# Performance work log

Measured on AMD Instinct MI355X. Metric: run time of the kernel, lower is better.

## Reference

```python
import math
import jax, jax.numpy as jnp
import numpy as np

D_SCALES = 4  # MSGAD d parameter


def calc_thetas(d):
    # Numeric replication of calculate_theta2 (beta-wavelet polynomial coeffs).
    # p_i(x) = (x/2)^i (1 - x/2)^(d-i) / (2 * Beta(i+1, d+1-i)); keep the d
    # lowest-order coefficients (constant .. x^{d-1}), matching the original.
    thetas = []
    for i in range(d):
        beta = math.factorial(i) * math.factorial(d - i) / math.factorial(d + 1)
        p = (np.poly1d([0.5, 0.0]) ** i) * (np.poly1d([-0.5, 1.0]) ** (d - i)) / (2.0 * beta)
        c = p.coeffs  # highest degree first, length d+1
        thetas.append([float(c[d - j]) for j in range(d)])
    return thetas

THETAS = calc_thetas(D_SCALES)


def setup_inputs() -> dict:
    key = jax.random.key(0)
    k1, k2, k3, k4 = jax.random.split(key, 4)
    N, E, IN, H = 8192, 262144, 256, 128
    in_feat = jax.random.normal(k1, (N, IN), dtype=jnp.float32)
    W = jax.random.normal(k2, (IN, H), dtype=jnp.float32) * 0.05
    b = jnp.zeros((H,), dtype=jnp.float32)
    src = jax.random.randint(k3, (E,), 0, N, dtype=jnp.int32)
    dst = jax.random.randint(k4, (E,), 0, N, dtype=jnp.int32)
    return {"in_feat": in_feat, "W": W, "b": b, "src": src, "dst": dst}


def reference(in_feat, W, b, src, dst):
    N = in_feat.shape[0]
    # Linear + LeakyReLU encoder
    h = jax.nn.leaky_relu(in_feat @ W + b, negative_slope=0.01)
    # dgl.add_self_loop
    loop = jnp.arange(N, dtype=src.dtype)
    s = jnp.concatenate([src, loop])
    d_ = jnp.concatenate([dst, loop])
    # out-degrees (with self loops), D^{-1/2} with clamp(min=1)
    deg = jax.ops.segment_sum(jnp.ones_like(s, dtype=jnp.float32), s, num_segments=N)
    dinv = jnp.maximum(deg, 1.0) ** -0.5  # [N]
    dinv = dinv[:, None]
    outs = []
    for theta in THETAS:
        feat = h
        acc = theta[0] * h
        for k in range(1, len(theta)):
            # unnormalized Laplacian: feat - D^{-1/2} A D^{-1/2} feat
            agg = jax.ops.segment_sum((feat * dinv)[s], d_, num_segments=N)
            feat = feat - agg * dinv
            acc = acc + theta[k] * feat
        outs.append(jnp.einsum('nd,md->nm', acc, acc))  # x @ x.T reconstruction
    return jnp.stack(outs)  # [d, N, N]
```

## Files before the change

### kernel.cpp

```cpp
#include <hip/hip_runtime.h>
#include <hip/hip_bf16.h>

#define N_NODES 8192
#define IN_DIM  256
#define H_DIM   128
#define N_EDGES 262144
#define BI 64
#define BJ 256

typedef __attribute__((ext_vector_type(8))) short bf16x8;
typedef __attribute__((ext_vector_type(4))) float f32x4;
typedef __attribute__((ext_vector_type(4))) short s16x4;

static __device__ inline short bf16_hi(float x) {
    __hip_bfloat16 h = __float2bfloat16(x);
    return *(short*)&h;
}
static __device__ inline float bf16_val(short s) {
    __hip_bfloat16 h = *(__hip_bfloat16*)&s;
    return __bfloat162float(h);
}

__global__ void hist_kernel(const int* __restrict__ src, const int* __restrict__ dst,
                            int* __restrict__ degc, int* __restrict__ dstc) {
    int e = blockIdx.x * 256 + threadIdx.x;
    if (e < N_EDGES) {
        atomicAdd(&degc[src[e]], 1);
        atomicAdd(&dstc[dst[e]], 1);
    }
}

__global__ void dinv_kernel(const int* __restrict__ degc, float* __restrict__ dinv) {
    int n = blockIdx.x * 256 + threadIdx.x;
    if (n < N_NODES) dinv[n] = 1.0f / sqrtf((float)(degc[n] + 1));
}

__global__ void scan_kernel(const int* __restrict__ cnt, int* __restrict__ rowptr,
                            int* __restrict__ cursor) {
    __shared__ int buf[2][256];
    int tid = threadIdx.x;
    const int chunk = N_NODES / 256;
    int base = tid * chunk;
    int s = 0;
    for (int i = 0; i < chunk; ++i) s += cnt[base + i];
    buf[0][tid] = s;
    __syncthreads();
    int pp = 0;
    for (int off = 1; off < 256; off <<= 1) {
        buf[pp ^ 1][tid] = buf[pp][tid] + (tid >= off ? buf[pp][tid - off] : 0);
        pp ^= 1;
        __syncthreads();
    }
    if (tid == 255) rowptr[N_NODES] = buf[pp][255];
    int run = buf[pp][tid] - s;
    for (int i = 0; i < chunk; ++i) {
        rowptr[base + i] = run;
        cursor[base + i] = run;
        run += cnt[base + i];
    }
}

__global__ void fill_kernel(const int* __restrict__ src, const int* __restrict__ dst,
                            int* __restrict__ cursor, int* __restrict__ colidx) {
    int e = blockIdx.x * 256 + threadIdx.x;
    if (e < N_EDGES) {
        int p = atomicAdd(&cursor[dst[e]], 1);
        colidx[p] = src[e];
    }
}

__global__ __launch_bounds__(256) void cvtX_kernel(const f32x4* __restrict__ X,
                                                   s16x4* __restrict__ Xhi,
                                                   s16x4* __restrict__ Xlo) {
    int i = blockIdx.x * 256 + threadIdx.x;
    f32x4 x = X[i];
    s16x4 hi, lo;
#pragma unroll
    for (int j = 0; j < 4; ++j) {
        short h = bf16_hi(x[j]);
        hi[j] = h;
        lo[j] = bf16_hi(x[j] - bf16_val(h));
    }
    Xhi[i] = hi;
    Xlo[i] = lo;
}

__global__ __launch_bounds__(256) void cvtW_kernel(const float* __restrict__ W,
                                                   short* __restrict__ Wthi,
                                                   short* __restrict__ Wtlo) {
    int t = blockIdx.x * 256 + threadIdx.x;
    int k = t & 255, j = t >> 8;
    float w = W[k * H_DIM + j];
    short h = bf16_hi(w);
    Wthi[t] = h;
    Wtlo[t] = bf16_hi(w - bf16_val(h));
}

__global__ __launch_bounds__(256) void gemm_h_mfma(const short* __restrict__ Xhi,
                                                   const short* __restrict__ Xlo,
                                                   const short* __restrict__ Wthi,
                                                   const short* __restrict__ Wtlo,
                                                   const float* __restrict__ b,
                                                   float* __restrict__ F0) {
    int lane = threadIdx.x & 63;
    int w    = threadIdx.x >> 6;
    int wr = w >> 1, wc = w & 1;
    int brow = blockIdx.x * 32 + wr * 16;
    int bcol = wc * 64;
    int r16 = lane & 15;
    int kg  = lane >> 4;

    f32x4 c[4] = {};
    for (int kk = 0; kk < IN_DIM / 32; ++kk) {
        int koff = kk * 32 + kg * 8;
        size_t aoff = (size_t)(brow + r16) * IN_DIM + koff;
        bf16x8 ah = *(const bf16x8*)(Xhi + aoff);
        bf16x8 al = *(const bf16x8*)(Xlo + aoff);
        bf16x8 bh[4], bl[4];
#pragma unroll
        for (int n = 0; n < 4; ++n) {
            size_t off = (size_t)(bcol + n * 16 + r16) * IN_DIM + koff;
            bh[n] = *(const bf16x8*)(Wthi + off);
            bl[n] = *(const bf16x8*)(Wtlo + off);
        }
#pragma unroll
        for (int n = 0; n < 4; ++n) {
            c[n] = __builtin_amdgcn_mfma_f32_16x16x32_bf16(ah, bh[n], c[n], 0, 0, 0);
            c[n] = __builtin_amdgcn_mfma_f32_16x16x32_bf16(ah, bl[n], c[n], 0, 0, 0);
            c[n] = __builtin_amdgcn_mfma_f32_16x16x32_bf16(al, bh[n], c[n], 0, 0, 0);
        }
    }
#pragma unroll
    for (int n = 0; n < 4; ++n)
#pragma unroll
        for (int r = 0; r < 4; ++r) {
            int row = brow + kg * 4 + r;
            int col = bcol + n * 16 + r16;
            float v = c[n][r] + b[col];
            v = v > 0.f ? v : 0.01f * v;
            F0[(size_t)row * H_DIM + col] = v;
        }
}

__global__ __launch_bounds__(128) void prop_kernel(const float* __restrict__ Fin,
                                                   float* __restrict__ Fout,
                                                   const float* __restrict__ dinv,
                                                   const int* __restrict__ rowptr,
                                                   const int* __restrict__ colidx) {
    int n = blockIdx.x;
    int j = threadIdx.x;
    float dv  = dinv[n];
    float fs  = Fin[(size_t)n * H_DIM + j];
    float sum = fs * dv;
    int beg = rowptr[n], end = rowptr[n + 1];
    int e = beg;
    for (; e + 4 <= end; e += 4) {
        int s0 = colidx[e], s1 = colidx[e + 1], s2 = colidx[e + 2], s3 = colidx[e + 3];
        float d0 = dinv[s0], d1 = dinv[s1], d2 = dinv[s2], d3 = dinv[s3];
        float v0 = Fin[(size_t)s0 * H_DIM + j];
        float v1 = Fin[(size_t)s1 * H_DIM + j];
        float v2 = Fin[(size_t)s2 * H_DIM + j];
        float v3 = Fin[(size_t)s3 * H_DIM + j];
        sum += v0 * d0 + v1 * d1 + v2 * d2 + v3 * d3;
    }
    for (; e < end; ++e) {
        int s0 = colidx[e];
        sum += Fin[(size_t)s0 * H_DIM + j] * dinv[s0];
    }
    Fout[(size_t)n * H_DIM + j] = fs - sum * dv;
}

__global__ __launch_bounds__(256) void acc_kernel(const f32x4* __restrict__ F0,
                                                  const f32x4* __restrict__ F1,
                                                  const f32x4* __restrict__ F2,
                                                  const f32x4* __restrict__ F3,
                                                  s16x4* __restrict__ accb) {
    int i = blockIdx.x * 256 + threadIdx.x;
    const size_t NH4 = (size_t)N_NODES * H_DIM / 4;
    f32x4 f0 = F0[i], f1 = F1[i], f2 = F2[i], f3 = F3[i];
    f32x4 a0 = 2.5f * f0 - 5.0f * f1 + 3.75f * f2 - 1.25f * f3;
    f32x4 a1 =           5.0f * f1 - 7.5f  * f2 + 3.75f * f3;
    f32x4 a2 =                      3.75f * f2 - 3.75f * f3;
    f32x4 a3 =                                   1.25f * f3;
    s16x4 o0, o1, o2, o3;
#pragma unroll
    for (int j = 0; j < 4; ++j) {
        o0[j] = bf16_hi(a0[j]); o1[j] = bf16_hi(a1[j]);
        o2[j] = bf16_hi(a2[j]); o3[j] = bf16_hi(a3[j]);
    }
    accb[0 * NH4 + i] = o0;
    accb[1 * NH4 + i] = o1;
    accb[2 * NH4 + i] = o2;
    accb[3 * NH4 + i] = o3;
}

__global__ __launch_bounds__(256) void out_gemm_kernel(const short* __restrict__ accb,
                                                       float* __restrict__ out) {
    __shared__ float lds[BI * BJ];
    int t = blockIdx.z;
    const short* A = accb + (size_t)t * N_NODES * H_DIM;
    int lane = threadIdx.x & 63;
    int w    = threadIdx.x >> 6;
    int ib = blockIdx.y * BI;
    int jb = blockIdx.x * BJ;
    int r16 = lane & 15;
    int kg  = lane >> 4;

    f32x4 c[4][4] = {};
    for (int kk = 0; kk < 4; ++kk) {
        int koff = kk * 32 + kg * 8;
        bf16x8 bi_f[4], aj_f[4];
#pragma unroll
        for (int n = 0; n < 4; ++n)
            bi_f[n] = *(const bf16x8*)(A + (size_t)(ib + n * 16 + r16) * H_DIM + koff);
#pragma unroll
        for (int m = 0; m < 4; ++m)
            aj_f[m] = *(const bf16x8*)(A + (size_t)(jb + w * 64 + m * 16 + r16) * H_DIM + koff);
#pragma unroll
        for (int m = 0; m < 4; ++m)
#pragma unroll
            for (int n = 0; n < 4; ++n)
                c[m][n] = __builtin_amdgcn_mfma_f32_16x16x32_bf16(aj_f[m], bi_f[n], c[m][n], 0, 0, 0);
    }

#pragma unroll
    for (int m = 0; m < 4; ++m)
#pragma unroll
        for (int n = 0; n < 4; ++n) {
            int i  = n * 16 + r16;
            int j  = w * 64 + m * 16 + kg * 4;
            int js = j ^ ((i & 7) << 2);
            *(f32x4*)(lds + i * BJ + js) = c[m][n];
        }
    __syncthreads();

    float* O = out + (size_t)t * N_NODES * N_NODES;
#pragma unroll
    for (int p = 0; p < 16; ++p) {
        int r  = p * 4 + w;
        f32x4 v = *(const f32x4*)(lds + r * BJ + lane * 4);
        int jl = (lane * 4) ^ ((r & 7) << 2);
        __builtin_nontemporal_store(v, (f32x4*)(O + (size_t)(ib + r) * N_NODES + jb + jl));
    }
}

extern "C" void kernel_launch(void* const* d_in, const int* in_sizes, int n_in,
                              void* d_out, int out_size, void* d_ws, size_t ws_size,
                              hipStream_t stream) {
    const float* in_feat = (const float*)d_in[0];
    const float* W       = (const float*)d_in[1];
    const float* b       = (const float*)d_in[2];
    const int*   src     = (const int*)d_in[3];
    const int*   dst     = (const int*)d_in[4];
    float* out = (float*)d_out;

    char* ws = (char*)d_ws;
    const size_t NH4 = (size_t)N_NODES * H_DIM * sizeof(float);
    float* F0 = (float*)(ws + 0 * NH4);
    float* F1 = (float*)(ws + 1 * NH4);
    float* F2 = (float*)(ws + 2 * NH4);
    float* F3 = (float*)(ws + 3 * NH4);
    char*  accb_region = ws + 4 * NH4;
    short* accb = (short*)accb_region;
    short* Xhi = (short*)accb_region;
    short* Xlo = (short*)(accb_region + NH4);
    char* p = ws + 6 * NH4;
    int*   degc   = (int*)p;   p += 32768;
    int*   dstc   = (int*)p;   p += 32768;
    float* dinv   = (float*)p; p += 32768;
    int*   rowptr = (int*)p;   p += 33792;
    int*   cursor = (int*)p;   p += 32768;
    int*   colidx = (int*)p;   p += (size_t)N_EDGES * 4;
    short* Wthi   = (short*)p; p += 65536;
    short* Wtlo   = (short*)p;

    hipMemsetAsync(degc, 0, 65536, stream);

    hist_kernel<<<N_EDGES / 256, 256, 0, stream>>>(src, dst, degc, dstc);
    dinv_kernel<<<N_NODES / 256, 256, 0, stream>>>(degc, dinv);
    scan_kernel<<<1, 256, 0, stream>>>(dstc, rowptr, cursor);
    fill_kernel<<<N_EDGES / 256, 256, 0, stream>>>(src, dst, cursor, colidx);

    cvtX_kernel<<<(N_NODES * IN_DIM / 4) / 256, 256, 0, stream>>>((const f32x4*)in_feat,
                                                                  (s16x4*)Xhi, (s16x4*)Xlo);
    cvtW_kernel<<<(H_DIM * IN_DIM) / 256, 256, 0, stream>>>(W, Wthi, Wtlo);

    gemm_h_mfma<<<N_NODES / 32, 256, 0, stream>>>(Xhi, Xlo, Wthi, Wtlo, b, F0);

    prop_kernel<<<N_NODES, 128, 0, stream>>>(F0, F1, dinv, rowptr, colidx);
    prop_kernel<<<N_NODES, 128, 0, stream>>>(F1, F2, dinv, rowptr, colidx);
    prop_kernel<<<N_NODES, 128, 0, stream>>>(F2, F3, dinv, rowptr, colidx);

    acc_kernel<<<(N_NODES * H_DIM / 4) / 256, 256, 0, stream>>>((const f32x4*)F0, (const f32x4*)F1,
                                                                (const f32x4*)F2, (const f32x4*)F3,
                                                                (s16x4*)accb);

    dim3 g(N_NODES / BJ, N_NODES / BI, 4);
    out_gemm_kernel<<<g, 256, 0, stream>>>(accb, out);
}
```

Before: 404.3 us.

## Shrink output tile, swizzle workgroup order, fuse small setup kernels

Halves the output GEMM tile height to 32 rows, giving twice as many workgroups with smaller LDS use, and launches them on a 1D grid with an XCD-style swizzle of block indices. The output stores switch from nontemporal to regular stores. The dinv computation is folded into the single-block scan kernel, and the X and W bf16 conversion kernels are merged into one launch, cutting launch overhead. The smaller tile lowers per-workgroup reuse of loaded operands, and the serial dinv loop adds work to the one-block scan.

```diff
diff --git a/kernel.cpp b/kernel.cpp
--- a/kernel.cpp
+++ b/kernel.cpp
@@ -5,7 +5,7 @@
 #define IN_DIM  256
 #define H_DIM   128
 #define N_EDGES 262144
-#define BI 64
+#define BI 32
 #define BJ 256
 
 typedef __attribute__((ext_vector_type(8))) short bf16x8;
@@ -30,19 +30,18 @@
     }
 }
 
-__global__ void dinv_kernel(const int* __restrict__ degc, float* __restrict__ dinv) {
-    int n = blockIdx.x * 256 + threadIdx.x;
-    if (n < N_NODES) dinv[n] = 1.0f / sqrtf((float)(degc[n] + 1));
-}
-
-__global__ void scan_kernel(const int* __restrict__ cnt, int* __restrict__ rowptr,
+__global__ void scan_kernel(const int* __restrict__ cnt, const int* __restrict__ degc,
+                            float* __restrict__ dinv, int* __restrict__ rowptr,
                             int* __restrict__ cursor) {
     __shared__ int buf[2][256];
     int tid = threadIdx.x;
     const int chunk = N_NODES / 256;
     int base = tid * chunk;
     int s = 0;
-    for (int i = 0; i < chunk; ++i) s += cnt[base + i];
+    for (int i = 0; i < chunk; ++i) {
+        s += cnt[base + i];
+        dinv[base + i] = 1.0f / sqrtf((float)(degc[base + i] + 1));
+    }
     buf[0][tid] = s;
     __syncthreads();
     int pp = 0;
@@ -69,31 +68,33 @@
     }
 }
 
-__global__ __launch_bounds__(256) void cvtX_kernel(const f32x4* __restrict__ X,
-                                                   s16x4* __restrict__ Xhi,
-                                                   s16x4* __restrict__ Xlo) {
-    int i = blockIdx.x * 256 + threadIdx.x;
-    f32x4 x = X[i];
-    s16x4 hi, lo;
-#pragma unroll
-    for (int j = 0; j < 4; ++j) {
-        short h = bf16_hi(x[j]);
-        hi[j] = h;
-        lo[j] = bf16_hi(x[j] - bf16_val(h));
-    }
-    Xhi[i] = hi;
-    Xlo[i] = lo;
-}
-
-__global__ __launch_bounds__(256) void cvtW_kernel(const float* __restrict__ W,
-                                                   short* __restrict__ Wthi,
-                                                   short* __restrict__ Wtlo) {
-    int t = blockIdx.x * 256 + threadIdx.x;
-    int k = t & 255, j = t >> 8;
-    float w = W[k * H_DIM + j];
-    short h = bf16_hi(w);
-    Wthi[t] = h;
-    Wtlo[t] = bf16_hi(w - bf16_val(h));
+__global__ __launch_bounds__(256) void cvt_kernel(const f32x4* __restrict__ X,
+                                                  s16x4* __restrict__ Xhi,
+                                                  s16x4* __restrict__ Xlo,
+                                                  const float* __restrict__ W,
+                                                  short* __restrict__ Wthi,
+                                                  short* __restrict__ Wtlo) {
+    int blk = blockIdx.x;
+    if (blk < 2048) {
+        int i = blk * 256 + threadIdx.x;
+        f32x4 x = X[i];
+        s16x4 hi, lo;
+#pragma unroll
+        for (int j = 0; j < 4; ++j) {
+            short h = bf16_hi(x[j]);
+            hi[j] = h;
+            lo[j] = bf16_hi(x[j] - bf16_val(h));
+        }
+        Xhi[i] = hi;
+        Xlo[i] = lo;
+    } else {
+        int t = (blk - 2048) * 256 + threadIdx.x;
+        int k = t & 255, j = t >> 8;
+        float w = W[k * H_DIM + j];
+        short h = bf16_hi(w);
+        Wthi[t] = h;
+        Wtlo[t] = bf16_hi(w - bf16_val(h));
+    }
 }
 
 __global__ __launch_bounds__(256) void gemm_h_mfma(const short* __restrict__ Xhi,
@@ -197,21 +198,30 @@
 __global__ __launch_bounds__(256) void out_gemm_kernel(const short* __restrict__ accb,
                                                        float* __restrict__ out) {
     __shared__ float lds[BI * BJ];
-    int t = blockIdx.z;
+    const int NJT = N_NODES / BJ;
+    const int NIT = N_NODES / BI;
+    const int NWG = NJT * NIT * 4;
+    int bid = blockIdx.x;
+    int swz  = (bid & 7) * (NWG >> 3) + (bid >> 3);
+    int xj   = swz % NJT;
+    int rest = swz / NJT;
+    int yi   = rest % NIT;
+    int t    = rest / NIT;
+
     const short* A = accb + (size_t)t * N_NODES * H_DIM;
     int lane = threadIdx.x & 63;
     int w    = threadIdx.x >> 6;
-    int ib = blockIdx.y * BI;
-    int jb = blockIdx.x * BJ;
+    int ib = yi * BI;
+    int jb = xj * BJ;
     int r16 = lane & 15;
     int kg  = lane >> 4;
 
-    f32x4 c[4][4] = {};
+    f32x4 c[4][2] = {};
     for (int kk = 0; kk < 4; ++kk) {
         int koff = kk * 32 + kg * 8;
-        bf16x8 bi_f[4], aj_f[4];
-#pragma unroll
-        for (int n = 0; n < 4; ++n)
+        bf16x8 bi_f[2], aj_f[4];
+#pragma unroll
+        for (int n = 0; n < 2; ++n)
             bi_f[n] = *(const bf16x8*)(A + (size_t)(ib + n * 16 + r16) * H_DIM + koff);
 #pragma unroll
         for (int m = 0; m < 4; ++m)
@@ -219,14 +229,14 @@
 #pragma unroll
         for (int m = 0; m < 4; ++m)
 #pragma unroll
-            for (int n = 0; n < 4; ++n)
+            for (int n = 0; n < 2; ++n)
                 c[m][n] = __builtin_amdgcn_mfma_f32_16x16x32_bf16(aj_f[m], bi_f[n], c[m][n], 0, 0, 0);
     }
 
 #pragma unroll
     for (int m = 0; m < 4; ++m)
 #pragma unroll
-        for (int n = 0; n < 4; ++n) {
+        for (int n = 0; n < 2; ++n) {
             int i  = n * 16 + r16;
             int j  = w * 64 + m * 16 + kg * 4;
             int js = j ^ ((i & 7) << 2);
@@ -236,11 +246,11 @@
 
     float* O = out + (size_t)t * N_NODES * N_NODES;
 #pragma unroll
-    for (int p = 0; p < 16; ++p) {
+    for (int p = 0; p < 8; ++p) {
         int r  = p * 4 + w;
         f32x4 v = *(const f32x4*)(lds + r * BJ + lane * 4);
         int jl = (lane * 4) ^ ((r & 7) << 2);
-        __builtin_nontemporal_store(v, (f32x4*)(O + (size_t)(ib + r) * N_NODES + jb + jl));
+        *(f32x4*)(O + (size_t)(ib + r) * N_NODES + jb + jl) = v;
     }
 }
 
@@ -277,13 +287,11 @@
     hipMemsetAsync(degc, 0, 65536, stream);
 
     hist_kernel<<<N_EDGES / 256, 256, 0, stream>>>(src, dst, degc, dstc);
-    dinv_kernel<<<N_NODES / 256, 256, 0, stream>>>(degc, dinv);
-    scan_kernel<<<1, 256, 0, stream>>>(dstc, rowptr, cursor);
+    scan_kernel<<<1, 256, 0, stream>>>(dstc, degc, dinv, rowptr, cursor);
     fill_kernel<<<N_EDGES / 256, 256, 0, stream>>>(src, dst, cursor, colidx);
 
-    cvtX_kernel<<<(N_NODES * IN_DIM / 4) / 256, 256, 0, stream>>>((const f32x4*)in_feat,
-                                                                  (s16x4*)Xhi, (s16x4*)Xlo);
-    cvtW_kernel<<<(H_DIM * IN_DIM) / 256, 256, 0, stream>>>(W, Wthi, Wtlo);
+    cvt_kernel<<<2048 + 128, 256, 0, stream>>>((const f32x4*)in_feat, (s16x4*)Xhi, (s16x4*)Xlo,
+                                               W, Wthi, Wtlo);
 
     gemm_h_mfma<<<N_NODES / 32, 256, 0, stream>>>(Xhi, Xlo, Wthi, Wtlo, b, F0);
 
@@ -295,6 +303,6 @@
                                                                 (const f32x4*)F2, (const f32x4*)F3,
                                                                 (s16x4*)accb);
 
-    dim3 g(N_NODES / BJ, N_NODES / BI, 4);
-    out_gemm_kernel<<<g, 256, 0, stream>>>(accb, out);
-}
+    const int NWG = (N_NODES / BJ) * (N_NODES / BI) * 4;
+    out_gemm_kernel<<<NWG, 256, 0, stream>>>(accb, out);
+}
```

New measurement: 517.5 us. +28.0%, slower.
